# Kernel tuning notes

Hardware: AMD Instinct MI355X
Metric: run time of the kernel (lower is better)

Reference implementation:

```python
import jax, jax.numpy as jnp
import numpy as np

NEG_INF = -100000000.0  # matches masked_fill value in torch source

def setup_inputs() -> dict:
    key = jax.random.key(0)
    ks = jax.random.split(key, 7)
    d_model, d = 1024, 128
    B, S = 4, 2048
    scale = 1.0 / np.sqrt(d_model)
    x = jax.random.normal(ks[0], (B, S, d_model), dtype=jnp.float32)
    Wq = jax.random.normal(ks[1], (d, d_model), dtype=jnp.float32) * scale
    bq = jax.random.normal(ks[2], (d,), dtype=jnp.float32) * 0.02
    Wk = jax.random.normal(ks[3], (d, d_model), dtype=jnp.float32) * scale
    bk = jax.random.normal(ks[4], (d,), dtype=jnp.float32) * 0.02
    Wv = jax.random.normal(ks[5], (d, d_model), dtype=jnp.float32) * scale
    bv = jax.random.normal(ks[6], (d,), dtype=jnp.float32) * 0.02
    return {"x": x, "Wq": Wq, "bq": bq, "Wk": Wk, "bk": bk, "Wv": Wv, "bv": bv}

def reference(x, Wq, bq, Wk, bk, Wv, bv):
    # Q,K,V: [B,S,d] via torch Linear (x @ W.T + b)
    Q = jnp.einsum('bsm,dm->bsd', x, Wq) + bq
    K = jnp.einsum('bsm,dm->bsd', x, Wk) + bk
    V = jnp.einsum('bsm,dm->bsd', x, Wv) + bv
    d = Wk.shape[0]
    scale = 1.0 / jnp.sqrt(jnp.asarray(d, dtype=Q.dtype))
    scores = jnp.einsum('bqd,bkd->bqk', Q, K) * scale  # [B,S,S]
    # Faithful to source: tril then value-based mask (tril==0 -> -1e8).
    tril = jnp.tril(scores)
    masked = jnp.where(tril == 0, NEG_INF, tril)
    attn = jax.nn.softmax(masked, axis=-1)
    context = jnp.einsum('bqk,bkd->bqd', attn, V)
    return context
```

## Files before the change

kernel.cpp:

```cpp
#include <hip/hip_runtime.h>

typedef __attribute__((ext_vector_type(8))) short bf16x8;
typedef __attribute__((ext_vector_type(4))) float f32x4;

__device__ __forceinline__ unsigned short f2bf(float f) {
    unsigned int u = __float_as_uint(f);
    u += 0x7fffu + ((u >> 16) & 1u);
    return (unsigned short)(u >> 16);
}
__device__ __forceinline__ unsigned int pack2bf(float lo, float hi) {
    return (unsigned int)f2bf(lo) | ((unsigned int)f2bf(hi) << 16);
}
__device__ __forceinline__ void async_ld16(void* lds, const void* g) {
    __builtin_amdgcn_global_load_lds(
        (const __attribute__((address_space(1))) unsigned int*)g,
        (__attribute__((address_space(3))) unsigned int*)lds, 16, 0, 0);
}

__global__ __launch_bounds__(256) void conv_w(
    const float* __restrict__ Wq, const float* __restrict__ Wk,
    const float* __restrict__ Wv, unsigned short* __restrict__ Wcat)
{
    size_t o = ((size_t)blockIdx.x * 256 + threadIdx.x) * 8;
    int sel = (int)(o >> 17);
    const float* W = (sel == 0) ? Wq : ((sel == 1) ? Wk : Wv);
    const float* src = W + (o & 131071);
    float4 f0 = ((const float4*)src)[0];
    float4 f1 = ((const float4*)src)[1];
    uint4 u;
    u.x = pack2bf(f0.x, f0.y); u.y = pack2bf(f0.z, f0.w);
    u.z = pack2bf(f1.x, f1.y); u.w = pack2bf(f1.z, f1.w);
    *(uint4*)(Wcat + o) = u;
}

__global__ __launch_bounds__(256) void qkv_gemm(
    const float* __restrict__ x,
    const unsigned short* __restrict__ Wcat,
    const float* __restrict__ bq, const float* __restrict__ bk,
    const float* __restrict__ bv,
    unsigned short* __restrict__ Qf,
    unsigned short* __restrict__ Kf,
    unsigned short* __restrict__ Vf)
{
    __shared__ unsigned short As[2][32 * 64];
    __shared__ unsigned short Bs[2][128 * 64];

    const int tid  = threadIdx.x;
    const int lane = tid & 63;
    const int w    = tid >> 6;
    const int quad = lane >> 4;
    const int ln   = lane & 15;
    const int lr   = lane >> 3;
    const int csw  = ((lane & 7) ^ lr) * 8;

    const int bid   = blockIdx.x;
    const int nb    = bid >> 8;
    const int mbase = (bid & 255) * 32;
    const unsigned short* Wsel = Wcat + (size_t)nb * 128 * 1024;

    const int arow  = tid >> 3;
    const int achk  = tid & 7;
    const int aslot = achk ^ (arow & 7);
    const float* xsrc = x + (size_t)(mbase + arow) * 1024 + achk * 8;
    unsigned short* adst0 = &As[0][arow * 64 + aslot * 8];
    unsigned short* adst1 = &As[1][arow * 64 + aslot * 8];

    f32x4 acc[2][2];
#pragma unroll
    for (int mt = 0; mt < 2; mt++)
#pragma unroll
        for (int nt = 0; nt < 2; nt++) acc[mt][nt] = (f32x4){0.f, 0.f, 0.f, 0.f};

    auto stageB = [&](int kb, int p) {
        const int kcol = kb * 64 + csw;
#pragma unroll
        for (int j = 0; j < 4; j++) {
            int chunk = w * 4 + j;
            async_ld16(&Bs[p][chunk * 512 + lane * 8],
                       Wsel + (size_t)(chunk * 8 + lr) * 1024 + kcol);
        }
    };
    auto writeA = [&](int p, const float4& f0, const float4& f1) {
        uint4 u;
        u.x = pack2bf(f0.x, f0.y); u.y = pack2bf(f0.z, f0.w);
        u.z = pack2bf(f1.x, f1.y); u.w = pack2bf(f1.z, f1.w);
        *(uint4*)((p == 0) ? adst0 : adst1) = u;
    };

    float4 a0 = ((const float4*)xsrc)[0];
    float4 a1 = ((const float4*)xsrc)[1];
    stageB(0, 0);
    writeA(0, a0, a1);
    __syncthreads();

    for (int kb = 0; kb < 16; kb++) {
        const int p = kb & 1;
        float4 n0, n1;
        if (kb < 15) {
            stageB(kb + 1, p ^ 1);
            const float* xs = xsrc + (kb + 1) * 64;
            n0 = ((const float4*)xs)[0];
            n1 = ((const float4*)xs)[1];
        }
#pragma unroll
        for (int ks = 0; ks < 2; ks++) {
            bf16x8 a[2], b[2];
#pragma unroll
            for (int mt = 0; mt < 2; mt++) {
                int row = mt * 16 + ln;
                a[mt] = *(const bf16x8*)&As[p][row * 64 + ((ks * 4 + quad) ^ (ln & 7)) * 8];
            }
#pragma unroll
            for (int nt = 0; nt < 2; nt++) {
                int row = w * 32 + nt * 16 + ln;
                b[nt] = *(const bf16x8*)&Bs[p][row * 64 + ((ks * 4 + quad) ^ (ln & 7)) * 8];
            }
#pragma unroll
            for (int mt = 0; mt < 2; mt++)
#pragma unroll
                for (int nt = 0; nt < 2; nt++)
                    acc[mt][nt] = __builtin_amdgcn_mfma_f32_16x16x32_bf16(
                        a[mt], b[nt], acc[mt][nt], 0, 0, 0);
        }
        if (kb < 15) writeA(p ^ 1, n0, n1);
        __syncthreads();
    }

    const float scale = (nb == 0) ? 0.08838834764831845f : 1.0f;
    const float* bsel = (nb == 0) ? bq : ((nb == 1) ? bk : bv);
    float bias_v[2];
#pragma unroll
    for (int nt = 0; nt < 2; nt++) bias_v[nt] = bsel[w * 32 + nt * 16 + ln];

    if (nb == 0) {
#pragma unroll
        for (int mt = 0; mt < 2; mt++)
#pragma unroll
            for (int nt = 0; nt < 2; nt++)
#pragma unroll
                for (int r = 0; r < 4; r++) {
                    int m = mbase + mt * 16 + quad * 4 + r;
                    int d = w * 32 + nt * 16 + ln;
                    int bb = m >> 11, s = m & 2047;
                    int qq = s >> 6, j = s & 63, wv = j >> 4, lnq = j & 15;
                    int ksd = d >> 5, rr = d & 31, qd = rr >> 3, e = rr & 7;
                    size_t idx = (((size_t)((bb * 32 + qq) * 4 + wv) * 4 + ksd) * 64
                                  + qd * 16 + lnq) * 8 + e;
                    Qf[idx] = f2bf((acc[mt][nt][r] + bias_v[nt]) * scale);
                }
    } else if (nb == 1) {
#pragma unroll
        for (int mt = 0; mt < 2; mt++)
#pragma unroll
            for (int nt = 0; nt < 2; nt++)
#pragma unroll
                for (int r = 0; r < 4; r++) {
                    int m = mbase + mt * 16 + quad * 4 + r;
                    int d = w * 32 + nt * 16 + ln;
                    int bb = m >> 11, s = m & 2047;
                    int kt = s >> 6, j = s & 63, ct = j >> 4, lnk = j & 15;
                    int ksd = d >> 5, rr = d & 31, qd = rr >> 3, e = rr & 7;
                    size_t idx = (((size_t)(bb * 128 + kt * 4 + ct) * 4 + ksd) * 64
                                  + qd * 16 + lnk) * 8 + e;
                    Kf[idx] = f2bf(acc[mt][nt][r] + bias_v[nt]);
                }
    } else {
#pragma unroll
        for (int mt = 0; mt < 2; mt++)
#pragma unroll
            for (int nt = 0; nt < 2; nt++) {
                int dd = w * 32 + nt * 16 + ln;
                int m0 = mbase + mt * 16 + quad * 4;
                int bb = m0 >> 11, s0 = m0 & 2047;
                int kt = s0 >> 6, j0 = s0 & 63;
                int kstep = j0 >> 5, rr0 = j0 & 31, qdv = rr0 >> 3, e0 = rr0 & 7;
                int dt = dd >> 4, lnv = dd & 15;
                size_t base = ((((size_t)(bb * 32 + kt) * 2 + kstep) * 8 + dt) * 64
                               + qdv * 16 + lnv) * 8 + e0;
                ushort4 u = { f2bf(acc[mt][nt][0] + bias_v[nt]),
                              f2bf(acc[mt][nt][1] + bias_v[nt]),
                              f2bf(acc[mt][nt][2] + bias_v[nt]),
                              f2bf(acc[mt][nt][3] + bias_v[nt]) };
                *(ushort4*)&Vf[base] = u;
            }
    }
}

__global__ __launch_bounds__(256) void flash_attn(
    const unsigned short* __restrict__ Qf,
    const unsigned short* __restrict__ Kf,
    const unsigned short* __restrict__ Vf,
    unsigned short* __restrict__ Opart,
    float* __restrict__ lsum_g)
{
    __shared__ unsigned short Pl[64][72];

    const int b = blockIdx.x;
    const int q = blockIdx.y;
    const int c = blockIdx.z;
    const int m4 = q >> 2, r4 = q & 3;
    if (c > m4) return;

    const int pbase = b * 144 + q + 2 * m4 * (m4 - 1) + r4 * m4;
    const int pidx  = pbase + c;
    const int k0 = c * 4;
    const int kend = (c * 4 + 4 < q + 1) ? (c * 4 + 4) : (q + 1);

    const int tid  = threadIdx.x;
    const int lane = tid & 63, w = tid >> 6, quad = lane >> 4, ln = lane & 15;
    const float M0 = 16.0f;

    bf16x8 qa[4];
    const unsigned short* qbt =
        Qf + (size_t)((b * 32 + q) * 4 + w) * 2048 + lane * 8;
#pragma unroll
    for (int ks = 0; ks < 4; ks++)
        qa[ks] = *(const bf16x8*)(qbt + (size_t)ks * 512);

    float l_i[4];
    f32x4 Ofr[8];
#pragma unroll
    for (int r = 0; r < 4; r++) l_i[r] = 0.f;
#pragma unroll
    for (int dt = 0; dt < 8; dt++) Ofr[dt] = (f32x4){0.f, 0.f, 0.f, 0.f};

    for (int kt = k0; kt < kend; kt++) {
        const unsigned short* kbt = Kf + (size_t)(b * 128 + kt * 4) * 2048 + lane * 8;
        const unsigned short* vbt = Vf + (size_t)(b * 32 + kt) * 8192 + lane * 8;
        bf16x8 kf[4][4], vf[2][8];
#pragma unroll
        for (int ct = 0; ct < 4; ct++)
#pragma unroll
            for (int ks = 0; ks < 4; ks++)
                kf[ct][ks] = *(const bf16x8*)(kbt + (size_t)(ct * 4 + ks) * 512);
#pragma unroll
        for (int kstep = 0; kstep < 2; kstep++)
#pragma unroll
            for (int dt = 0; dt < 8; dt++)
                vf[kstep][dt] = *(const bf16x8*)(vbt + (size_t)(kstep * 8 + dt) * 512);

        f32x4 sfr[4];
#pragma unroll
        for (int ct = 0; ct < 4; ct++) {
            f32x4 s = (f32x4){0.f, 0.f, 0.f, 0.f};
#pragma unroll
            for (int ks = 0; ks < 4; ks++)
                s = __builtin_amdgcn_mfma_f32_16x16x32_bf16(qa[ks], kf[ct][ks], s, 0, 0, 0);
            sfr[ct] = s;
        }

        if (kt == q) {
#pragma unroll
            for (int ct = 0; ct < 4; ct++)
#pragma unroll
                for (int r = 0; r < 4; r++)
                    if (ct * 16 + ln > w * 16 + quad * 4 + r)
                        sfr[ct][r] = -__builtin_inff();
        }

#pragma unroll
        for (int ct = 0; ct < 4; ct++)
#pragma unroll
            for (int r = 0; r < 4; r++) {
                float pv = __expf(sfr[ct][r] - M0);
                l_i[r] += pv;
                Pl[w * 16 + quad * 4 + r][ct * 16 + ln] = f2bf(pv);
            }

#pragma unroll
        for (int kstep = 0; kstep < 2; kstep++) {
            bf16x8 pa = *(const bf16x8*)&Pl[w * 16 + ln][kstep * 32 + quad * 8];
#pragma unroll
            for (int dt = 0; dt < 8; dt++)
                Ofr[dt] = __builtin_amdgcn_mfma_f32_16x16x32_bf16(pa, vf[kstep][dt], Ofr[dt], 0, 0, 0);
        }
    }

#pragma unroll
    for (int off = 1; off < 16; off <<= 1)
#pragma unroll
        for (int r = 0; r < 4; r++) l_i[r] += __shfl_xor(l_i[r], off, 64);

#pragma unroll
    for (int dt = 0; dt < 8; dt++)
#pragma unroll
        for (int r = 0; r < 4; r++) {
            int row = w * 16 + quad * 4 + r;
            Opart[((size_t)pidx * 64 + row) * 128 + dt * 16 + ln] = f2bf(Ofr[dt][r]);
        }
    if (ln == 0) {
#pragma unroll
        for (int r = 0; r < 4; r++) {
            int row = w * 16 + quad * 4 + r;
            lsum_g[(size_t)pidx * 64 + row] = l_i[r];
        }
    }
}

__global__ __launch_bounds__(256) void combine(
    const unsigned short* __restrict__ Opart,
    const float* __restrict__ lsum_g,
    float* __restrict__ out)
{
    const int idx  = blockIdx.x >> 1;
    const int half = blockIdx.x & 1;
    const int b = idx >> 5, q = idx & 31;
    const int m4 = q >> 2, r4 = q & 3;
    const int pbase = b * 144 + q + 2 * m4 * (m4 - 1) + r4 * m4;
    const int nc = m4 + 1;

    const int row = threadIdx.x & 63;
    const int grp = half * 64 + (threadIdx.x >> 6) * 16;

    float lsum = 0.f;
#pragma unroll
    for (int c2 = 0; c2 < 8; c2++) {
        int cc = (c2 < nc) ? c2 : (nc - 1);
        float lc = lsum_g[(size_t)(pbase + cc) * 64 + row];
        lsum += (c2 < nc) ? lc : 0.f;
    }
    const float inv = 1.0f / lsum;

#pragma unroll
    for (int v = 0; v < 2; v++) {
        int col = grp + v * 8;
        float acc[8];
#pragma unroll
        for (int k = 0; k < 8; k++) acc[k] = 0.f;
#pragma unroll
        for (int c2 = 0; c2 < 8; c2++) {
            int cc = (c2 < nc) ? c2 : (nc - 1);
            uint4 u = *(const uint4*)&Opart[((size_t)(pbase + cc) * 64 + row) * 128 + col];
            float wc = (c2 < nc) ? 1.f : 0.f;
            acc[0] += wc * __uint_as_float(u.x << 16);
            acc[1] += wc * __uint_as_float(u.x & 0xffff0000u);
            acc[2] += wc * __uint_as_float(u.y << 16);
            acc[3] += wc * __uint_as_float(u.y & 0xffff0000u);
            acc[4] += wc * __uint_as_float(u.z << 16);
            acc[5] += wc * __uint_as_float(u.z & 0xffff0000u);
            acc[6] += wc * __uint_as_float(u.w << 16);
            acc[7] += wc * __uint_as_float(u.w & 0xffff0000u);
        }
        float* o = &out[((size_t)b * 2048 + q * 64 + row) * 128 + col];
        float4 o0 = { acc[0] * inv, acc[1] * inv, acc[2] * inv, acc[3] * inv };
        float4 o1 = { acc[4] * inv, acc[5] * inv, acc[6] * inv, acc[7] * inv };
        ((float4*)o)[0] = o0;
        ((float4*)o)[1] = o1;
    }
}

extern "C" void kernel_launch(void* const* d_in, const int* in_sizes, int n_in,
                              void* d_out, int out_size, void* d_ws, size_t ws_size,
                              hipStream_t stream) {
    const float* x  = (const float*)d_in[0];
    const float* Wq = (const float*)d_in[1];
    const float* bq = (const float*)d_in[2];
    const float* Wk = (const float*)d_in[3];
    const float* bk = (const float*)d_in[4];
    const float* Wv = (const float*)d_in[5];
    const float* bv = (const float*)d_in[6];
    float* out = (float*)d_out;

    char* wsb = (char*)d_ws;
    unsigned short* Opart = (unsigned short*)wsb;
    float*          lsum  = (float*)(wsb + 9437184);
    unsigned short* Wcat  = (unsigned short*)(wsb + 10485760);
    unsigned short* Qf    = (unsigned short*)(wsb + 11272192);
    unsigned short* Kf    = Qf + (size_t)8192 * 128;
    unsigned short* Vf    = Qf + (size_t)2 * 8192 * 128;

    conv_w<<<192, 256, 0, stream>>>(Wq, Wk, Wv, Wcat);
    qkv_gemm<<<768, 256, 0, stream>>>(x, Wcat, bq, bk, bv, Qf, Kf, Vf);
    flash_attn<<<dim3(4, 32, 8), 256, 0, stream>>>(Qf, Kf, Vf, Opart, lsum);
    combine<<<256, 256, 0, stream>>>(Opart, lsum, out);
}
```

Baseline: 123.3 us.

## Fuse split-KV combine into attention via last-block atomic ticket reduction

Removes the separate combine kernel: each attention block writes its bf16 partial output and row sums, takes an atomic ticket per query tile, and the last-arriving block reduces all partials and writes the normalized fp32 output. Tiles with a single chunk write the output directly. The grid becomes a compact 1D launch of only the valid blocks instead of a 3D grid with early-exit blocks, and the partial layout is changed to fragment-contiguous vector stores. It adds threadfences, an atomic per block, and a serial reduction tail in the last block, plus a counter reset placed in conv_w.

New measurement: 212.6 us. 1.72x slower.

```diff
diff --git a/kernel.cpp b/kernel.cpp
--- a/kernel.cpp
+++ b/kernel.cpp
@@ -8,6 +8,9 @@
     u += 0x7fffu + ((u >> 16) & 1u);
     return (unsigned short)(u >> 16);
 }
+__device__ __forceinline__ float bf2f(unsigned short h) {
+    return __uint_as_float((unsigned int)h << 16);
+}
 __device__ __forceinline__ unsigned int pack2bf(float lo, float hi) {
     return (unsigned int)f2bf(lo) | ((unsigned int)f2bf(hi) << 16);
 }
@@ -19,8 +22,10 @@
 
 __global__ __launch_bounds__(256) void conv_w(
     const float* __restrict__ Wq, const float* __restrict__ Wk,
-    const float* __restrict__ Wv, unsigned short* __restrict__ Wcat)
+    const float* __restrict__ Wv, unsigned short* __restrict__ Wcat,
+    int* __restrict__ cnt)
 {
+    if (blockIdx.x == 0 && threadIdx.x < 128) cnt[threadIdx.x] = 0;
     size_t o = ((size_t)blockIdx.x * 256 + threadIdx.x) * 8;
     int sel = (int)(o >> 17);
     const float* W = (sel == 0) ? Wq : ((sel == 1) ? Wk : Wv);
@@ -186,21 +191,30 @@
     }
 }
 
-__global__ __launch_bounds__(256) void flash_attn(
+__global__ __launch_bounds__(256) void flash_fused(
     const unsigned short* __restrict__ Qf,
     const unsigned short* __restrict__ Kf,
     const unsigned short* __restrict__ Vf,
     unsigned short* __restrict__ Opart,
-    float* __restrict__ lsum_g)
+    float* __restrict__ lsum_g,
+    int* __restrict__ cnt,
+    float* __restrict__ out)
 {
     __shared__ unsigned short Pl[64][72];
-
-    const int b = blockIdx.x;
-    const int q = blockIdx.y;
-    const int c = blockIdx.z;
+    __shared__ int sTicket;
+
+    int j = blockIdx.x;
+    const int b = j / 144;
+    int t = j % 144;
+    int q = 0, c = 0;
+#pragma unroll 1
+    for (int qq = 0; qq < 32; qq++) {
+        int ncq = (qq >> 2) + 1;
+        if (t < ncq) { q = qq; c = t; break; }
+        t -= ncq;
+    }
     const int m4 = q >> 2, r4 = q & 3;
-    if (c > m4) return;
-
+    const int nc = m4 + 1;
     const int pbase = b * 144 + q + 2 * m4 * (m4 - 1) + r4 * m4;
     const int pidx  = pbase + c;
     const int k0 = c * 4;
@@ -281,71 +295,68 @@
 #pragma unroll
         for (int r = 0; r < 4; r++) l_i[r] += __shfl_xor(l_i[r], off, 64);
 
-#pragma unroll
-    for (int dt = 0; dt < 8; dt++)
-#pragma unroll
-        for (int r = 0; r < 4; r++) {
-            int row = w * 16 + quad * 4 + r;
-            Opart[((size_t)pidx * 64 + row) * 128 + dt * 16 + ln] = f2bf(Ofr[dt][r]);
-        }
+    auto writeOut = [&](const float* inv_) {
+#pragma unroll
+        for (int dt = 0; dt < 8; dt++)
+#pragma unroll
+            for (int r = 0; r < 4; r++) {
+                int row = w * 16 + quad * 4 + r;
+                out[((size_t)(b * 2048 + q * 64 + row)) * 128 + dt * 16 + ln] =
+                    Ofr[dt][r] * inv_[r];
+            }
+    };
+
+    if (nc == 1) {
+        float inv_[4];
+#pragma unroll
+        for (int r = 0; r < 4; r++) inv_[r] = 1.0f / l_i[r];
+        writeOut(inv_);
+        return;
+    }
+
+#pragma unroll
+    for (int dt = 0; dt < 8; dt++) {
+        ushort4 u = { f2bf(Ofr[dt][0]), f2bf(Ofr[dt][1]),
+                      f2bf(Ofr[dt][2]), f2bf(Ofr[dt][3]) };
+        *(ushort4*)&Opart[(((size_t)pidx * 8 + dt) * 4 + w) * 256 + lane * 4] = u;
+    }
     if (ln == 0) {
 #pragma unroll
-        for (int r = 0; r < 4; r++) {
-            int row = w * 16 + quad * 4 + r;
-            lsum_g[(size_t)pidx * 64 + row] = l_i[r];
-        }
-    }
-}
-
-__global__ __launch_bounds__(256) void combine(
-    const unsigned short* __restrict__ Opart,
-    const float* __restrict__ lsum_g,
-    float* __restrict__ out)
-{
-    const int idx  = blockIdx.x >> 1;
-    const int half = blockIdx.x & 1;
-    const int b = idx >> 5, q = idx & 31;
-    const int m4 = q >> 2, r4 = q & 3;
-    const int pbase = b * 144 + q + 2 * m4 * (m4 - 1) + r4 * m4;
-    const int nc = m4 + 1;
-
-    const int row = threadIdx.x & 63;
-    const int grp = half * 64 + (threadIdx.x >> 6) * 16;
-
-    float lsum = 0.f;
-#pragma unroll
-    for (int c2 = 0; c2 < 8; c2++) {
-        int cc = (c2 < nc) ? c2 : (nc - 1);
-        float lc = lsum_g[(size_t)(pbase + cc) * 64 + row];
-        lsum += (c2 < nc) ? lc : 0.f;
-    }
-    const float inv = 1.0f / lsum;
-
-#pragma unroll
-    for (int v = 0; v < 2; v++) {
-        int col = grp + v * 8;
-        float acc[8];
-#pragma unroll
-        for (int k = 0; k < 8; k++) acc[k] = 0.f;
-#pragma unroll
-        for (int c2 = 0; c2 < 8; c2++) {
-            int cc = (c2 < nc) ? c2 : (nc - 1);
-            uint4 u = *(const uint4*)&Opart[((size_t)(pbase + cc) * 64 + row) * 128 + col];
-            float wc = (c2 < nc) ? 1.f : 0.f;
-            acc[0] += wc * __uint_as_float(u.x << 16);
-            acc[1] += wc * __uint_as_float(u.x & 0xffff0000u);
-            acc[2] += wc * __uint_as_float(u.y << 16);
-            acc[3] += wc * __uint_as_float(u.y & 0xffff0000u);
-            acc[4] += wc * __uint_as_float(u.z << 16);
-            acc[5] += wc * __uint_as_float(u.z & 0xffff0000u);
-            acc[6] += wc * __uint_as_float(u.w << 16);
-            acc[7] += wc * __uint_as_float(u.w & 0xffff0000u);
-        }
-        float* o = &out[((size_t)b * 2048 + q * 64 + row) * 128 + col];
-        float4 o0 = { acc[0] * inv, acc[1] * inv, acc[2] * inv, acc[3] * inv };
-        float4 o1 = { acc[4] * inv, acc[5] * inv, acc[6] * inv, acc[7] * inv };
-        ((float4*)o)[0] = o0;
-        ((float4*)o)[1] = o1;
+        for (int r = 0; r < 4; r++)
+            lsum_g[(size_t)pidx * 64 + w * 16 + quad * 4 + r] = l_i[r];
+    }
+
+    __threadfence();
+    __syncthreads();
+    if (tid == 0) sTicket = atomicAdd(&cnt[b * 32 + q], 1);
+    __syncthreads();
+
+    if (sTicket == nc - 1) {
+        __threadfence();
+        float lt[4];
+#pragma unroll
+        for (int r = 0; r < 4; r++) lt[r] = l_i[r];
+
+#pragma unroll 1
+        for (int c2 = 0; c2 < nc; c2++) {
+            if (c2 == c) continue;
+            const size_t pb2 = (size_t)(pbase + c2);
+#pragma unroll
+            for (int r = 0; r < 4; r++)
+                lt[r] += lsum_g[pb2 * 64 + w * 16 + quad * 4 + r];
+#pragma unroll
+            for (int dt = 0; dt < 8; dt++) {
+                ushort4 u = *(const ushort4*)&Opart[((pb2 * 8 + dt) * 4 + w) * 256 + lane * 4];
+                Ofr[dt][0] += bf2f(u.x);
+                Ofr[dt][1] += bf2f(u.y);
+                Ofr[dt][2] += bf2f(u.z);
+                Ofr[dt][3] += bf2f(u.w);
+            }
+        }
+        float inv_[4];
+#pragma unroll
+        for (int r = 0; r < 4; r++) inv_[r] = 1.0f / lt[r];
+        writeOut(inv_);
     }
 }
 
@@ -364,13 +375,13 @@
     char* wsb = (char*)d_ws;
     unsigned short* Opart = (unsigned short*)wsb;
     float*          lsum  = (float*)(wsb + 9437184);
+    int*            cnt   = (int*)(wsb + 9600000);
     unsigned short* Wcat  = (unsigned short*)(wsb + 10485760);
     unsigned short* Qf    = (unsigned short*)(wsb + 11272192);
     unsigned short* Kf    = Qf + (size_t)8192 * 128;
     unsigned short* Vf    = Qf + (size_t)2 * 8192 * 128;
 
-    conv_w<<<192, 256, 0, stream>>>(Wq, Wk, Wv, Wcat);
+    conv_w<<<192, 256, 0, stream>>>(Wq, Wk, Wv, Wcat, cnt);
     qkv_gemm<<<768, 256, 0, stream>>>(x, Wcat, bq, bk, bv, Qf, Kf, Vf);
-    flash_attn<<<dim3(4, 32, 8), 256, 0, stream>>>(Qf, Kf, Vf, Opart, lsum);
-    combine<<<256, 256, 0, stream>>>(Opart, lsum, out);
-}
+    flash_fused<<<576, 256, 0, stream>>>(Qf, Kf, Vf, Opart, lsum, cnt, out);
+}
```
